# Performance work log

Hardware: AMD Instinct MI355X
Metric: run time of the kernel (lower is better)

The kernel has to match this reference:

```python
import jax, jax.numpy as jnp
import numpy as np

N_NODES = 50000
N_EDGES = 800000
IN_DIM = 128
HEADS = 8
F_OUT = 16


def setup_inputs() -> dict:
    key = jax.random.key(0)
    ks = jax.random.split(key, 7)
    x = jax.random.normal(ks[0], (N_NODES, IN_DIM), dtype=jnp.float32)
    edge_index = jax.random.randint(ks[1], (2, N_EDGES), 0, N_NODES, dtype=jnp.int32)
    # xavier-normal-ish scale
    W_proj = jax.random.normal(ks[2], (HEADS * F_OUT, IN_DIM), dtype=jnp.float32) * (2.0 / (IN_DIM + HEADS * F_OUT)) ** 0.5
    a_src = jax.random.normal(ks[3], (HEADS, F_OUT), dtype=jnp.float32) * 0.1
    a_tgt = jax.random.normal(ks[4], (HEADS, F_OUT), dtype=jnp.float32) * 0.1
    W_skip = jax.random.normal(ks[5], (HEADS * F_OUT, IN_DIM), dtype=jnp.float32) * (2.0 / (IN_DIM + HEADS * F_OUT)) ** 0.5
    bias = jnp.zeros((HEADS * F_OUT,), dtype=jnp.float32)
    return {"x": x, "edge_index": edge_index, "W_proj": W_proj, "a_src": a_src,
            "a_tgt": a_tgt, "W_skip": W_skip, "bias": bias}


def reference(x, edge_index, W_proj, a_src, a_tgt, W_skip, bias):
    N = x.shape[0]
    src, tgt = edge_index[0], edge_index[1]
    # project: [N, H, F]
    proj = (x @ W_proj.T).reshape(N, HEADS, F_OUT)
    # per-node partial scores: [N, H]
    s_src = jnp.einsum('nhf,hf->nh', proj, a_src)
    s_tgt = jnp.einsum('nhf,hf->nh', proj, a_tgt)
    # per-edge scores, LeakyReLU(0.2): [E, H]
    e = jax.nn.leaky_relu(s_src[src] + s_tgt[tgt], negative_slope=0.2)
    # segment softmax over incoming edges of each target node
    e_max = jax.ops.segment_max(e, tgt, num_segments=N)
    e_exp = jnp.exp(e - e_max[tgt])
    denom = jax.ops.segment_sum(e_exp, tgt, num_segments=N)
    alpha = e_exp / (denom[tgt] + 1e-16)  # [E, H]
    # weighted scatter-add of projected source features: [N, H, F]
    msgs = proj[src] * alpha[:, :, None]
    out = jax.ops.segment_sum(msgs, tgt, num_segments=N)
    # skip connection (in_dim != out_dim path -> skip_proj), concat heads, bias, ELU
    out = out + (x @ W_skip.T).reshape(N, HEADS, F_OUT)
    out = out.reshape(N, HEADS * F_OUT) + bias
    return jax.nn.elu(out)
```

## Files before the change

### kernel.cpp

```cpp
#include <hip/hip_runtime.h>
#include <hip/hip_bf16.h>
#include <math.h>

#define PADN 50048
#define CAP 64
#define NBIN 98
#define BINSZ 512
#define SEGCAP 9216
#define EPB 8192
#define INVALID 0xFFFFFFFFu

typedef __attribute__((ext_vector_type(8))) short short8;
typedef __attribute__((ext_vector_type(4))) float f32x4;
typedef __attribute__((ext_vector_type(4))) unsigned int uint4v;

__device__ __forceinline__ unsigned short f2b(float f) {
  __hip_bfloat16 h = __float2bfloat16(f);
  return *(unsigned short*)&h;
}

__global__ __launch_bounds__(256) void k_init(const float* __restrict__ Wp,
                                              const float* __restrict__ Ws,
                                              const float* __restrict__ a_src,
                                              const float* __restrict__ a_tgt,
                                              unsigned short* __restrict__ Bpk,
                                              int* __restrict__ cursor) {
  const int b = blockIdx.x;
  if (b == 17) {
    if (threadIdx.x < NBIN) cursor[threadIdx.x] = threadIdx.x * SEGCAP;
    return;
  }
  int idx = b * 256 + threadIdx.x;
  int tile = idx >> 8;
  int ks = (idx >> 6) & 3;
  int lane = idx & 63;
  int kbase = ks * 32 + (lane >> 4) * 8;
  unsigned short o[8];
  if (tile < 16) {
    int col = tile * 16 + (lane & 15);
    const float* src = (col < 128) ? (Wp + (size_t)col * 128 + kbase)
                                   : (Ws + (size_t)(col - 128) * 128 + kbase);
#pragma unroll
    for (int j = 0; j < 8; ++j) o[j] = f2b(src[j]);
  } else {
    int col = lane & 15;
    int h = col & 7;
    const float* av = (col < 8) ? (a_src + h * 16) : (a_tgt + h * 16);
#pragma unroll
    for (int j = 0; j < 8; ++j) {
      int k = kbase + j;
      float s = 0.f;
#pragma unroll
      for (int f = 0; f < 16; ++f) s = fmaf(Wp[(size_t)(h * 16 + f) * 128 + k], av[f], s);
      o[j] = f2b(s);
    }
  }
  *(short8*)(Bpk + (size_t)idx * 8) = *(short8*)o;
}

__global__ __launch_bounds__(256) void k_pg(
    const float* __restrict__ x, const unsigned short* __restrict__ Bpk,
    unsigned short* __restrict__ pb, unsigned short* __restrict__ sb,
    float* __restrict__ ssrc, float* __restrict__ stgt,
    const int* __restrict__ ei, int* __restrict__ cursor,
    unsigned int* __restrict__ binned, int N, int E, int partB) {
  __shared__ unsigned int ord[EPB];
  __shared__ int hist_w[4][128];
  __shared__ int woff_[4][128];
  __shared__ int posw_[4][128];
  __shared__ int base_[128], scn[128], mybase[128];
  const int b = blockIdx.x;
  if (b < partB) {
    const int tid = threadIdx.x;
    const int wv = tid >> 6;
    const int e0 = b * EPB;
    const int ne = min(EPB, E - e0);
    const int* srcp = ei;
    const int* tgtp = ei + E;
    for (int i = tid; i < 512; i += 256) {
      ((int*)hist_w)[i] = 0;
      ((int*)posw_)[i] = 0;
    }
    __syncthreads();
    unsigned int pk[32];
#pragma unroll
    for (int j = 0; j < 8; ++j) {
      int e4 = e0 + (j * 256 + tid) * 4;
      if (e4 < E) {
        uint4v t4 = *(const uint4v*)(tgtp + e4);
        uint4v s4 = *(const uint4v*)(srcp + e4);
#pragma unroll
        for (int k = 0; k < 4; ++k) {
          pk[j * 4 + k] = (t4[k] << 16) | s4[k];
          atomicAdd(&hist_w[wv][t4[k] >> 9], 1);
        }
      } else {
#pragma unroll
        for (int k = 0; k < 4; ++k) pk[j * 4 + k] = INVALID;
      }
    }
    __syncthreads();
    if (tid < 128) {
      int w0 = hist_w[0][tid], w1 = hist_w[1][tid];
      int w2 = hist_w[2][tid], w3 = hist_w[3][tid];
      woff_[0][tid] = 0;
      woff_[1][tid] = w0;
      woff_[2][tid] = w0 + w1;
      woff_[3][tid] = w0 + w1 + w2;
      scn[tid] = w0 + w1 + w2 + w3;
    }
    __syncthreads();
    int c = (tid < 128) ? scn[tid] : 0;
#pragma unroll
    for (int off = 1; off < 128; off <<= 1) {
      int v = 0;
      if (tid < 128 && tid >= off) v = scn[tid - off];
      __syncthreads();
      if (tid < 128) scn[tid] += v;
      __syncthreads();
    }
    if (tid < 128) {
      base_[tid] = scn[tid] - c;
      mybase[tid] = (tid < NBIN && c > 0) ? atomicAdd(&cursor[tid], c) : 0;
    }
    __syncthreads();
#pragma unroll
    for (int j = 0; j < 32; ++j) {
      if (pk[j] != INVALID) {
        int bb = pk[j] >> 25;
        int r = atomicAdd(&posw_[wv][bb], 1);
        ord[base_[bb] + woff_[wv][bb] + r] = pk[j];
      }
    }
    __syncthreads();
    for (int i = tid; i < ne; i += 256) {
      unsigned int p = ord[i];
      int bb = p >> 25;
      int gpos = mybase[bb] + (i - base_[bb]);
      if (gpos < (bb + 1) * SEGCAP) binned[gpos] = p;
    }
    return;
  }

  const int wave = threadIdx.x >> 6, lane = threadIdx.x & 63;
  const int m = lane & 15, q = lane >> 4;
  const int r0 = (b - partB) * 128 + wave * 32;

  short8 a[2][4];
#pragma unroll
  for (int g = 0; g < 2; ++g) {
    const int row_a = r0 + g * 16 + m;
#pragma unroll
    for (int ks = 0; ks < 4; ++ks) {
      float4 v0 = make_float4(0.f, 0.f, 0.f, 0.f), v1 = v0;
      if (row_a < N) {
        const float4* xp = (const float4*)(x + (size_t)row_a * 128 + ks * 32 + q * 8);
        v0 = xp[0];
        v1 = xp[1];
      }
      unsigned short o[8];
      o[0] = f2b(v0.x); o[1] = f2b(v0.y); o[2] = f2b(v0.z); o[3] = f2b(v0.w);
      o[4] = f2b(v1.x); o[5] = f2b(v1.y); o[6] = f2b(v1.z); o[7] = f2b(v1.w);
      a[g][ks] = *(short8*)o;
    }
  }

#define LOADB(dst, t)                                                        \
  {                                                                          \
    const unsigned short* bp_ = Bpk + (size_t)((t) * 256 + lane) * 8;        \
    dst[0] = *(const short8*)(bp_ + 0 * 512);                                \
    dst[1] = *(const short8*)(bp_ + 1 * 512);                                \
    dst[2] = *(const short8*)(bp_ + 2 * 512);                                \
    dst[3] = *(const short8*)(bp_ + 3 * 512);                                \
  }

  short8 bb[2][4];
  LOADB(bb[0], 0)
#pragma unroll
  for (int ct = 0; ct < 17; ++ct) {
    if (ct < 16) LOADB(bb[(ct + 1) & 1], ct + 1)
    f32x4 acc0 = {0.f, 0.f, 0.f, 0.f};
    f32x4 acc1 = {0.f, 0.f, 0.f, 0.f};
#pragma unroll
    for (int ks = 0; ks < 4; ++ks) {
      acc0 = __builtin_amdgcn_mfma_f32_16x16x32_bf16(a[0][ks], bb[ct & 1][ks], acc0, 0, 0, 0);
      acc1 = __builtin_amdgcn_mfma_f32_16x16x32_bf16(a[1][ks], bb[ct & 1][ks], acc1, 0, 0, 0);
    }
    if (ct < 16) {
      unsigned short* dst = (ct < 8) ? pb : sb;
      const int cc = (ct & 7) * 16 + m;
#pragma unroll
      for (int r = 0; r < 4; ++r) {
        int row0 = r0 + q * 4 + r;
        if (row0 < N) dst[(size_t)row0 * 128 + cc] = f2b(acc0[r]);
        int row1 = r0 + 16 + q * 4 + r;
        if (row1 < N) dst[(size_t)row1 * 128 + cc] = f2b(acc1[r]);
      }
    } else {
      float* sd = (m < 8) ? ssrc : stgt;
      const int h = m & 7;
#pragma unroll
      for (int r = 0; r < 4; ++r) {
        int row0 = r0 + q * 4 + r;
        if (row0 < N) sd[row0 * 8 + h] = acc0[r];
        int row1 = r0 + 16 + q * 4 + r;
        if (row1 < N) sd[row1 * 8 + h] = acc1[r];
      }
    }
  }
#undef LOADB
}

__global__ __launch_bounds__(256) void k_csr(const unsigned int* __restrict__ binned,
                                             const int* __restrict__ cursor,
                                             int* __restrict__ counts,
                                             unsigned short* __restrict__ esrc,
                                             int N) {
  __shared__ unsigned short buck[128 * CAP];
  __shared__ int cnt128[128];
  const int g = blockIdx.x >> 2, qq = blockIdx.x & 3, tid = threadIdx.x;
  const int lo = g * BINSZ + qq * 128;
  for (int i = tid; i < 128; i += 256) cnt128[i] = 0;
  __syncthreads();
  const int cnt = min(cursor[g] - g * SEGCAP, SEGCAP);
  const unsigned int* seg = binned + (size_t)g * SEGCAP;
  const int c4 = cnt >> 2;
  for (int i = tid; i < c4; i += 256) {
    uint4v p4 = *(const uint4v*)(seg + i * 4);
#pragma unroll
    for (int k = 0; k < 4; ++k) {
      unsigned int p = p4[k];
      int tl = (p >> 16) & (BINSZ - 1);
      if ((tl >> 7) == qq) {
        int r = atomicAdd(&cnt128[tl & 127], 1);
        if (r < CAP) buck[((tl & 127) << 6) + r] = (unsigned short)(p & 0xFFFFu);
      }
    }
  }
  for (int i = c4 * 4 + tid; i < cnt; i += 256) {
    unsigned int p = seg[i];
    int tl = (p >> 16) & (BINSZ - 1);
    if ((tl >> 7) == qq) {
      int r = atomicAdd(&cnt128[tl & 127], 1);
      if (r < CAP) buck[((tl & 127) << 6) + r] = (unsigned short)(p & 0xFFFFu);
    }
  }
  __syncthreads();
  uint4* dst = (uint4*)(esrc + ((size_t)lo << 6));
  const uint4* s4 = (const uint4*)buck;
  for (int v = tid; v < (128 * CAP) / 8; v += 256) dst[v] = s4[v];
  for (int i = tid; i < 128; i += 256) {
    int n = lo + i;
    if (n < N) counts[n] = min(cnt128[i], CAP);
  }
}

__global__ __launch_bounds__(256) void k_agg(const unsigned short* __restrict__ pb,
                                             const unsigned short* __restrict__ sb,
                                             const float* __restrict__ ssrc,
                                             const float* __restrict__ stgt,
                                             const float* __restrict__ bias,
                                             const int* __restrict__ counts,
                                             const unsigned short* __restrict__ esrc,
                                             float* __restrict__ out, int N) {
  __shared__ float w_lds[4][64 * 9];
  int wid = (int)((blockIdx.x * (size_t)blockDim.x + threadIdx.x) >> 6);
  int lane = threadIdx.x & 63;
  if (wid >= N) return;
  const int n = wid;
  const int wv = threadIdx.x >> 6;
  const int c = lane * 2;
  const int h = lane >> 3;

  const int cnt = min(counts[n], CAP);
  const int srcv = (int)esrc[(n << 6) + lane];

  {
    const bool val = lane < cnt;
    const int s_safe = val ? srcv : 0;
    const float4* sp = (const float4*)(ssrc + s_safe * 8);
    float4 s01 = sp[0], s23 = sp[1];
    const float4* tp = (const float4*)(stgt + n * 8);
    float4 t01 = tp[0], t23 = tp[1];
    float w[8];
    w[0] = s01.x + t01.x; w[1] = s01.y + t01.y;
    w[2] = s01.z + t01.z; w[3] = s01.w + t01.w;
    w[4] = s23.x + t23.x; w[5] = s23.y + t23.y;
    w[6] = s23.z + t23.z; w[7] = s23.w + t23.w;
#pragma unroll
    for (int k = 0; k < 8; ++k) {
      float e_ = fmaxf(w[k], 0.2f * w[k]);
      w[k] = val ? __expf(e_) : 0.0f;
    }
    float* wr = &w_lds[wv][lane * 9];
#pragma unroll
    for (int k = 0; k < 8; ++k) wr[k] = w[k];
  }

  float ds0 = 0.f, ds1 = 0.f, ds2 = 0.f, ds3 = 0.f;
  float x00 = 0.f, x01 = 0.f, x10 = 0.f, x11 = 0.f;
  float x20 = 0.f, x21 = 0.f, x30 = 0.f, x31 = 0.f;

#define LOADP(p, jj)                                                   \
  {                                                                    \
    int s_ = __builtin_amdgcn_readlane(srcv, min((jj), cm));           \
    pv##p = *(const unsigned int*)(pb + (size_t)s_ * 128 + c);         \
  }
#define CONS(p, dsx, a0x, a1x, jj)                                     \
  {                                                                    \
    float w_ = w_lds[wv][(jj) * 9 + h];                                \
    dsx += w_;                                                         \
    a0x = fmaf(w_, __uint_as_float(pv##p << 16), a0x);                 \
    a1x = fmaf(w_, __uint_as_float(pv##p & 0xffff0000u), a1x);         \
  }

  const int p8 = (cnt + 7) & ~7;
  if (p8 > 0) {
    const int cm = cnt - 1;
    unsigned int pv0, pv1, pv2, pv3, pv4, pv5, pv6, pv7;
    LOADP(0, 0) LOADP(1, 1) LOADP(2, 2) LOADP(3, 3)
    LOADP(4, 4) LOADP(5, 5) LOADP(6, 6) LOADP(7, 7)
    for (int j = 0; j + 8 <= p8; j += 8) {
      CONS(0, ds0, x00, x01, j + 0)
      CONS(1, ds1, x10, x11, j + 1)
      CONS(2, ds2, x20, x21, j + 2)
      CONS(3, ds3, x30, x31, j + 3)
      if (j + 8 < p8) {
        LOADP(0, j + 8) LOADP(1, j + 9) LOADP(2, j + 10) LOADP(3, j + 11)
      }
      CONS(4, ds0, x00, x01, j + 4)
      CONS(5, ds1, x10, x11, j + 5)
      CONS(6, ds2, x20, x21, j + 6)
      CONS(7, ds3, x30, x31, j + 7)
      if (j + 8 < p8) {
        LOADP(4, j + 12) LOADP(5, j + 13) LOADP(6, j + 14) LOADP(7, j + 15)
      }
    }
  }
#undef LOADP
#undef CONS

  const float dsum = (ds0 + ds1) + (ds2 + ds3);
  const float acc0 = (x00 + x10) + (x20 + x30);
  const float acc1 = (x01 + x11) + (x21 + x31);
  const float inv = 1.0f / (dsum + 1e-16f);
  size_t row = (size_t)n * 128;
  unsigned int su = *(const unsigned int*)(sb + row + c);
  float sk0 = __uint_as_float(su << 16);
  float sk1 = __uint_as_float(su & 0xffff0000u);
  float r0 = fmaf(acc0, inv, sk0) + bias[c];
  float r1 = fmaf(acc1, inv, sk1) + bias[c + 1];
  r0 = (r0 > 0.f) ? r0 : (__expf(r0) - 1.0f);
  r1 = (r1 > 0.f) ? r1 : (__expf(r1) - 1.0f);
  *(float2*)(out + row + c) = make_float2(r0, r1);
}

extern "C" void kernel_launch(void* const* d_in, const int* in_sizes, int n_in,
                              void* d_out, int out_size, void* d_ws, size_t ws_size,
                              hipStream_t stream) {
  const float* x = (const float*)d_in[0];
  const int* ei = (const int*)d_in[1];
  const float* Wp = (const float*)d_in[2];
  const float* a_src = (const float*)d_in[3];
  const float* a_tgt = (const float*)d_in[4];
  const float* Ws = (const float*)d_in[5];
  const float* bias = (const float*)d_in[6];
  float* out = (float*)d_out;

  const int N = in_sizes[0] / 128;
  const int E = in_sizes[1] / 2;

  unsigned short* Bpk = (unsigned short*)d_ws;
  unsigned short* pb = Bpk + 34816;
  unsigned short* sb = pb + (size_t)N * 128;
  float* ssrc = (float*)(sb + (size_t)N * 128);
  float* stgt = ssrc + (size_t)N * 8;
  int* counts = (int*)(stgt + (size_t)N * 8);
  unsigned short* esrcU = (unsigned short*)(counts + N);
  unsigned int* binned = (unsigned int*)(esrcU + (size_t)NBIN * BINSZ * CAP);
  int* cursor = (int*)(binned + (size_t)NBIN * SEGCAP);

  const int partB = (E + EPB - 1) / EPB;
  const int gemmB = PADN / 128;

  k_init<<<18, 256, 0, stream>>>(Wp, Ws, a_src, a_tgt, Bpk, cursor);
  k_pg<<<partB + gemmB, 256, 0, stream>>>(x, Bpk, pb, sb, ssrc, stgt, ei, cursor,
                                          binned, N, E, partB);
  k_csr<<<NBIN * 4, 256, 0, stream>>>(binned, cursor, counts, esrcU, N);
  k_agg<<<(N + 3) / 4, 256, 0, stream>>>(pb, sb, ssrc, stgt, bias, counts, esrcU, out, N);
}
```

Baseline: 154.1 us.

## Split projection GEMM across partition and CSR kernels; halve edges per block

```diff
diff --git a/kernel.cpp b/kernel.cpp
--- a/kernel.cpp
+++ b/kernel.cpp
@@ -7,7 +7,7 @@
 #define NBIN 98
 #define BINSZ 512
 #define SEGCAP 9216
-#define EPB 8192
+#define EPB 4096
 #define INVALID 0xFFFFFFFFu
 
 typedef __attribute__((ext_vector_type(8))) short short8;
@@ -17,6 +17,81 @@
 __device__ __forceinline__ unsigned short f2b(float f) {
   __hip_bfloat16 h = __float2bfloat16(f);
   return *(unsigned short*)&h;
+}
+
+__device__ void gemm_block(const float* __restrict__ x,
+                           const unsigned short* __restrict__ Bpk,
+                           unsigned short* __restrict__ pb,
+                           unsigned short* __restrict__ sb,
+                           float* __restrict__ ssrc, float* __restrict__ stgt,
+                           int N, int rowBase, int tid) {
+  const int wave = tid >> 6, lane = tid & 63;
+  const int m = lane & 15, q = lane >> 4;
+  const int r0 = rowBase + wave * 32;
+
+  short8 a[2][4];
+#pragma unroll
+  for (int g = 0; g < 2; ++g) {
+    const int row_a = r0 + g * 16 + m;
+#pragma unroll
+    for (int ks = 0; ks < 4; ++ks) {
+      float4 v0 = make_float4(0.f, 0.f, 0.f, 0.f), v1 = v0;
+      if (row_a < N) {
+        const float4* xp = (const float4*)(x + (size_t)row_a * 128 + ks * 32 + q * 8);
+        v0 = xp[0];
+        v1 = xp[1];
+      }
+      unsigned short o[8];
+      o[0] = f2b(v0.x); o[1] = f2b(v0.y); o[2] = f2b(v0.z); o[3] = f2b(v0.w);
+      o[4] = f2b(v1.x); o[5] = f2b(v1.y); o[6] = f2b(v1.z); o[7] = f2b(v1.w);
+      a[g][ks] = *(short8*)o;
+    }
+  }
+
+#define LOADB(dst, t)                                                        \
+  {                                                                          \
+    const unsigned short* bp_ = Bpk + (size_t)((t) * 256 + lane) * 8;        \
+    dst[0] = *(const short8*)(bp_ + 0 * 512);                                \
+    dst[1] = *(const short8*)(bp_ + 1 * 512);                                \
+    dst[2] = *(const short8*)(bp_ + 2 * 512);                                \
+    dst[3] = *(const short8*)(bp_ + 3 * 512);                                \
+  }
+
+  short8 bb[2][4];
+  LOADB(bb[0], 0)
+#pragma unroll
+  for (int ct = 0; ct < 17; ++ct) {
+    if (ct < 16) LOADB(bb[(ct + 1) & 1], ct + 1)
+    f32x4 acc0 = {0.f, 0.f, 0.f, 0.f};
+    f32x4 acc1 = {0.f, 0.f, 0.f, 0.f};
+#pragma unroll
+    for (int ks = 0; ks < 4; ++ks) {
+      acc0 = __builtin_amdgcn_mfma_f32_16x16x32_bf16(a[0][ks], bb[ct & 1][ks], acc0, 0, 0, 0);
+      acc1 = __builtin_amdgcn_mfma_f32_16x16x32_bf16(a[1][ks], bb[ct & 1][ks], acc1, 0, 0, 0);
+    }
+    if (ct < 16) {
+      unsigned short* dst = (ct < 8) ? pb : sb;
+      const int cc = (ct & 7) * 16 + m;
+#pragma unroll
+      for (int r = 0; r < 4; ++r) {
+        int row0 = r0 + q * 4 + r;
+        if (row0 < N) dst[(size_t)row0 * 128 + cc] = f2b(acc0[r]);
+        int row1 = r0 + 16 + q * 4 + r;
+        if (row1 < N) dst[(size_t)row1 * 128 + cc] = f2b(acc1[r]);
+      }
+    } else {
+      float* sd = (m < 8) ? ssrc : stgt;
+      const int h = m & 7;
+#pragma unroll
+      for (int r = 0; r < 4; ++r) {
+        int row0 = r0 + q * 4 + r;
+        if (row0 < N) sd[row0 * 8 + h] = acc0[r];
+        int row1 = r0 + 16 + q * 4 + r;
+        if (row1 < N) sd[row1 * 8 + h] = acc1[r];
+      }
+    }
+  }
+#undef LOADB
 }
 
 __global__ __launch_bounds__(256) void k_init(const float* __restrict__ Wp,
@@ -82,9 +157,9 @@
       ((int*)posw_)[i] = 0;
     }
     __syncthreads();
-    unsigned int pk[32];
-#pragma unroll
-    for (int j = 0; j < 8; ++j) {
+    unsigned int pk[16];
+#pragma unroll
+    for (int j = 0; j < 4; ++j) {
       int e4 = e0 + (j * 256 + tid) * 4;
       if (e4 < E) {
         uint4v t4 = *(const uint4v*)(tgtp + e4);
@@ -125,7 +200,7 @@
     }
     __syncthreads();
 #pragma unroll
-    for (int j = 0; j < 32; ++j) {
+    for (int j = 0; j < 16; ++j) {
       if (pk[j] != INVALID) {
         int bb = pk[j] >> 25;
         int r = atomicAdd(&posw_[wv][bb], 1);
@@ -141,84 +216,29 @@
     }
     return;
   }
-
-  const int wave = threadIdx.x >> 6, lane = threadIdx.x & 63;
-  const int m = lane & 15, q = lane >> 4;
-  const int r0 = (b - partB) * 128 + wave * 32;
-
-  short8 a[2][4];
-#pragma unroll
-  for (int g = 0; g < 2; ++g) {
-    const int row_a = r0 + g * 16 + m;
-#pragma unroll
-    for (int ks = 0; ks < 4; ++ks) {
-      float4 v0 = make_float4(0.f, 0.f, 0.f, 0.f), v1 = v0;
-      if (row_a < N) {
-        const float4* xp = (const float4*)(x + (size_t)row_a * 128 + ks * 32 + q * 8);
-        v0 = xp[0];
-        v1 = xp[1];
-      }
-      unsigned short o[8];
-      o[0] = f2b(v0.x); o[1] = f2b(v0.y); o[2] = f2b(v0.z); o[3] = f2b(v0.w);
-      o[4] = f2b(v1.x); o[5] = f2b(v1.y); o[6] = f2b(v1.z); o[7] = f2b(v1.w);
-      a[g][ks] = *(short8*)o;
-    }
-  }
-
-#define LOADB(dst, t)                                                        \
-  {                                                                          \
-    const unsigned short* bp_ = Bpk + (size_t)((t) * 256 + lane) * 8;        \
-    dst[0] = *(const short8*)(bp_ + 0 * 512);                                \
-    dst[1] = *(const short8*)(bp_ + 1 * 512);                                \
-    dst[2] = *(const short8*)(bp_ + 2 * 512);                                \
-    dst[3] = *(const short8*)(bp_ + 3 * 512);                                \
-  }
-
-  short8 bb[2][4];
-  LOADB(bb[0], 0)
-#pragma unroll
-  for (int ct = 0; ct < 17; ++ct) {
-    if (ct < 16) LOADB(bb[(ct + 1) & 1], ct + 1)
-    f32x4 acc0 = {0.f, 0.f, 0.f, 0.f};
-    f32x4 acc1 = {0.f, 0.f, 0.f, 0.f};
-#pragma unroll
-    for (int ks = 0; ks < 4; ++ks) {
-      acc0 = __builtin_amdgcn_mfma_f32_16x16x32_bf16(a[0][ks], bb[ct & 1][ks], acc0, 0, 0, 0);
-      acc1 = __builtin_amdgcn_mfma_f32_16x16x32_bf16(a[1][ks], bb[ct & 1][ks], acc1, 0, 0, 0);
-    }
-    if (ct < 16) {
-      unsigned short* dst = (ct < 8) ? pb : sb;
-      const int cc = (ct & 7) * 16 + m;
-#pragma unroll
-      for (int r = 0; r < 4; ++r) {
-        int row0 = r0 + q * 4 + r;
-        if (row0 < N) dst[(size_t)row0 * 128 + cc] = f2b(acc0[r]);
-        int row1 = r0 + 16 + q * 4 + r;
-        if (row1 < N) dst[(size_t)row1 * 128 + cc] = f2b(acc1[r]);
-      }
-    } else {
-      float* sd = (m < 8) ? ssrc : stgt;
-      const int h = m & 7;
-#pragma unroll
-      for (int r = 0; r < 4; ++r) {
-        int row0 = r0 + q * 4 + r;
-        if (row0 < N) sd[row0 * 8 + h] = acc0[r];
-        int row1 = r0 + 16 + q * 4 + r;
-        if (row1 < N) sd[row1 * 8 + h] = acc1[r];
-      }
-    }
-  }
-#undef LOADB
+  gemm_block(x, Bpk, pb, sb, ssrc, stgt, N, (b - partB) * 128, threadIdx.x);
 }
 
 __global__ __launch_bounds__(256) void k_csr(const unsigned int* __restrict__ binned,
                                              const int* __restrict__ cursor,
                                              int* __restrict__ counts,
                                              unsigned short* __restrict__ esrc,
-                                             int N) {
+                                             const float* __restrict__ x,
+                                             const unsigned short* __restrict__ Bpk,
+                                             unsigned short* __restrict__ pb,
+                                             unsigned short* __restrict__ sb,
+                                             float* __restrict__ ssrc,
+                                             float* __restrict__ stgt,
+                                             int N, int csrB, int rowBase) {
   __shared__ unsigned short buck[128 * CAP];
   __shared__ int cnt128[128];
-  const int g = blockIdx.x >> 2, qq = blockIdx.x & 3, tid = threadIdx.x;
+  const int blk = blockIdx.x;
+  if (blk >= csrB) {
+    gemm_block(x, Bpk, pb, sb, ssrc, stgt, N, rowBase + (blk - csrB) * 128,
+               threadIdx.x);
+    return;
+  }
+  const int g = blk >> 2, qq = blk & 3, tid = threadIdx.x;
   const int lo = g * BINSZ + qq * 128;
   for (int i = tid; i < 128; i += 256) cnt128[i] = 0;
   __syncthreads();
@@ -382,10 +402,15 @@
 
   const int partB = (E + EPB - 1) / EPB;
   const int gemmB = PADN / 128;
+  const int gemmB1 = 196;
+  const int gemmB2 = gemmB - gemmB1;
+  const int csrB = NBIN * 4;
 
   k_init<<<18, 256, 0, stream>>>(Wp, Ws, a_src, a_tgt, Bpk, cursor);
-  k_pg<<<partB + gemmB, 256, 0, stream>>>(x, Bpk, pb, sb, ssrc, stgt, ei, cursor,
-                                          binned, N, E, partB);
-  k_csr<<<NBIN * 4, 256, 0, stream>>>(binned, cursor, counts, esrcU, N);
+  k_pg<<<partB + gemmB1, 256, 0, stream>>>(x, Bpk, pb, sb, ssrc, stgt, ei, cursor,
+                                           binned, N, E, partB);
+  k_csr<<<csrB + gemmB2, 256, 0, stream>>>(binned, cursor, counts, esrcU,
+                                           x, Bpk, pb, sb, ssrc, stgt,
+                                           N, csrB, gemmB1 * 128);
   k_agg<<<(N + 3) / 4, 256, 0, stream>>>(pb, sb, ssrc, stgt, bias, counts, esrcU, out, N);
 }
```

Result: slower. 158.7 us (+3.0%).
